# Performance work log

Measured on AMD Instinct MI355X. Metric: run time of the kernel, lower is better.

## Reference

```python
import jax, jax.numpy as jnp
import numpy as np

K = 512
DIM = 256
BETA = 0.25


def setup_inputs() -> dict:
    key = jax.random.key(0)
    k1, k2 = jax.random.split(key)
    x = jax.random.normal(k1, (64, DIM, 32, 32), dtype=jnp.float32)
    lookup_table = jax.random.normal(k2, (K, DIM), dtype=jnp.float32)
    return {"x": x, "lookup_table": lookup_table}


def reference(x, lookup_table):
    b, d, h, w = x.shape
    # [b,d,h,w] -> [b*h*w, d]
    xf = jnp.transpose(x, (0, 2, 3, 1)).reshape(-1, d)
    # Squared Euclidean distances (argmin identical to torch.cdist argmin)
    d2 = (
        jnp.sum(xf * xf, axis=-1, keepdims=True)
        - 2.0 * (xf @ lookup_table.T)
        + jnp.sum(lookup_table * lookup_table, axis=-1)
    )  # [N, K]
    q = jnp.argmin(d2, axis=1)  # [N]
    x_e = lookup_table[q].reshape(b, h, w, d).transpose(0, 3, 1, 2)  # [b,d,h,w]
    q_x = q.reshape(b, h, w)
    codebook_loss = jnp.mean(jnp.square(jax.lax.stop_gradient(x) - x_e))
    commitment_loss = jnp.mean(jnp.square(x - jax.lax.stop_gradient(x_e)))
    loss = codebook_loss + BETA * commitment_loss
    return x_e, q_x, loss
```

## Files before the change

### kernel.cpp

```cpp
#include <hip/hip_runtime.h>

#define DIM     256
#define HW      1024
#define N_ROWS  65536
#define NT      512
#define QBM     128
#define NBLK    512
#define MARGIN  0.0625f

#define OUT_Q_OFF    16777216
#define OUT_LOSS_OFF 16842752

#define WS_DIST   512
#define WS_X2     1024
#define WS_CNT_I  1536
#define WS_LIST_I 2048
#define WS_LUTBF_B 524288

typedef __attribute__((ext_vector_type(8))) short short8v;
typedef __attribute__((ext_vector_type(4))) float floatx4;

__device__ __forceinline__ unsigned short bf16_rne(float f) {
    unsigned int u = __float_as_uint(f);
    u += 0x7fffu + ((u >> 16) & 1u);
    return (unsigned short)(u >> 16);
}
__device__ __forceinline__ float bf16_to_f(unsigned short h) {
    return __uint_as_float(((unsigned int)h) << 16);
}
__device__ __forceinline__ uint4 pack8(const unsigned short* h) {
    uint4 u;
    u.x = (unsigned)h[0] | ((unsigned)h[1] << 16);
    u.y = (unsigned)h[2] | ((unsigned)h[3] << 16);
    u.z = (unsigned)h[4] | ((unsigned)h[5] << 16);
    u.w = (unsigned)h[6] | ((unsigned)h[7] << 16);
    return u;
}

__global__ void c2_kernel(const float* __restrict__ lut, float* __restrict__ ws) {
    if (threadIdx.x == 0) ((int*)ws)[WS_CNT_I] = 0;
    int t = threadIdx.x;
    for (int k = t; k < 512; k += 256) {
        const float4* row = (const float4*)(lut + (size_t)k * DIM);
        float s = 0.f;
        #pragma unroll 8
        for (int i = 0; i < DIM / 4; ++i) {
            float4 v = row[i];
            s += v.x * v.x + v.y * v.y + v.z * v.z + v.w * v.w;
        }
        ws[k] = s;
    }
}

__global__ void lutprep_kernel(const float* __restrict__ lut, float* __restrict__ ws) {
    int g = blockIdx.x * 256 + threadIdx.x;
    int lane = g & 63;
    int ctg  = (g >> 6) & 31;
    int dcg  = g >> 11;
    int code = ctg * 16 + (lane & 15);
    int d0   = dcg * 32 + (lane >> 4) * 8;
    const float* src = lut + (size_t)code * DIM + d0;
    unsigned short hi[8], lo[8];
    #pragma unroll
    for (int j = 0; j < 8; ++j) {
        float v = src[j];
        unsigned short h = bf16_rne(v);
        hi[j] = h;
        lo[j] = bf16_rne(v - bf16_to_f(h));
    }
    char* dst = (char*)ws + WS_LUTBF_B + (size_t)((dcg * 32 + ctg) * 2) * 1024 + lane * 16;
    *(uint4*)dst          = pack8(hi);
    *(uint4*)(dst + 1024) = pack8(lo);
}

__global__ __launch_bounds__(NT, 2) void vq_kernel(const float* __restrict__ x,
                                                   const float* __restrict__ lut,
                                                   float* __restrict__ out,
                                                   float* __restrict__ ws) {
    __shared__ uint4 aS4[1024];
    __shared__ float c2s[512];
    __shared__ float redv1[4][QBM];
    __shared__ float redv2[4][QBM];
    __shared__ int   redi1[4][QBM];
    __shared__ int   qsh[QBM];
    __shared__ float wsumd[2];
    __shared__ float wsumx[8];

    char* aS = (char*)aS4;
    const char* lutbf = (const char*)ws + WS_LUTBF_B;

    const int tid = threadIdx.x;
    const int blk = blockIdx.x;
    const int n0  = blk * QBM;
    const int b   = n0 >> 10;
    const int hw0 = n0 & 1023;
    const float* xb = x + (size_t)b * (DIM * HW) + hw0;

    for (int k = tid; k < 512; k += NT) c2s[k] = ws[k];

    const int wave = tid >> 6;
    const int lane = tid & 63;
    const int l15  = lane & 15;
    const int l4   = lane >> 4;
    const int rg   = wave >> 2;
    const int cg   = wave & 3;

    const int srow   = tid & 127;
    const int schunk = tid >> 7;
    const int srt    = srow >> 4;
    const int slf    = schunk * 16 + (srow & 15);

    float x2local = 0.f;
    floatx4 acc[4][8];
    #pragma unroll
    for (int i = 0; i < 4; ++i)
        #pragma unroll
        for (int j = 0; j < 8; ++j) acc[i][j] = (floatx4)0.f;

    for (int dc = 0; dc < 8; ++dc) {
        __syncthreads();
        {
            const float* src = xb + (size_t)(dc * 32 + schunk * 8) * HW + srow;
            unsigned short hi[8], lo[8];
            #pragma unroll
            for (int j = 0; j < 8; ++j) {
                float v = src[(size_t)j * HW];
                x2local = fmaf(v, v, x2local);
                unsigned short h = bf16_rne(v);
                hi[j] = h;
                lo[j] = bf16_rne(v - bf16_to_f(h));
            }
            *(uint4*)(aS + srt * 1024 + slf * 16)        = pack8(hi);
            *(uint4*)(aS + 8192 + srt * 1024 + slf * 16) = pack8(lo);
        }
        __syncthreads();
        short8v ah[4], al[4];
        #pragma unroll
        for (int rtl = 0; rtl < 4; ++rtl) {
            ah[rtl] = *(const short8v*)(aS + (rg * 4 + rtl) * 1024 + lane * 16);
            al[rtl] = *(const short8v*)(aS + 8192 + (rg * 4 + rtl) * 1024 + lane * 16);
        }
        #pragma unroll
        for (int ct = 0; ct < 8; ++ct) {
            const char* bp = lutbf + (size_t)((dc * 32 + cg * 8 + ct) * 2) * 1024 + lane * 16;
            short8v bh = *(const short8v*)bp;
            short8v bl = *(const short8v*)(bp + 1024);
            #pragma unroll
            for (int rtl = 0; rtl < 4; ++rtl) {
                acc[rtl][ct] = __builtin_amdgcn_mfma_f32_16x16x32_bf16(ah[rtl], bh, acc[rtl][ct], 0, 0, 0);
                acc[rtl][ct] = __builtin_amdgcn_mfma_f32_16x16x32_bf16(al[rtl], bh, acc[rtl][ct], 0, 0, 0);
                acc[rtl][ct] = __builtin_amdgcn_mfma_f32_16x16x32_bf16(ah[rtl], bl, acc[rtl][ct], 0, 0, 0);
            }
        }
    }

    #pragma unroll
    for (int rtl = 0; rtl < 4; ++rtl) {
        #pragma unroll
        for (int r = 0; r < 4; ++r) {
            float v1 = 3.4e38f, v2 = 3.4e38f; int i1 = 0;
            #pragma unroll
            for (int ct = 0; ct < 8; ++ct) {
                int code = cg * 128 + ct * 16 + l15;
                float dist = fmaf(-2.f, acc[rtl][ct][r], c2s[code]);
                if (dist < v1) { v2 = v1; v1 = dist; i1 = code; }
                else if (dist < v2) v2 = dist;
            }
            #pragma unroll
            for (int off = 1; off < 16; off <<= 1) {
                float ov1 = __shfl_xor(v1, off, 64);
                int   oi1 = __shfl_xor(i1, off, 64);
                float ov2 = __shfl_xor(v2, off, 64);
                float nv2 = fminf(fmaxf(v1, ov1), fminf(v2, ov2));
                if (ov1 < v1 || (ov1 == v1 && oi1 < i1)) { v1 = ov1; i1 = oi1; }
                v2 = nv2;
            }
            if (l15 == 0) {
                int row = rg * 64 + rtl * 16 + l4 * 4 + r;
                redv1[cg][row] = v1; redi1[cg][row] = i1; redv2[cg][row] = v2;
            }
        }
    }
    __syncthreads();

    float dist_part = 0.f;
    if (tid < QBM) {
        const int row = tid;
        float v1 = redv1[0][row]; int i1 = redi1[0][row]; float v2 = redv2[0][row];
        #pragma unroll
        for (int s = 1; s < 4; ++s) {
            float ov1 = redv1[s][row]; int oi1 = redi1[s][row]; float ov2 = redv2[s][row];
            float nv2 = fminf(fmaxf(v1, ov1), fminf(v2, ov2));
            if (ov1 < v1 || (ov1 == v1 && oi1 < i1)) { v1 = ov1; i1 = oi1; }
            v2 = nv2;
        }
        qsh[row] = i1;
        out[OUT_Q_OFF + n0 + row] = (float)i1;
        if (v2 - v1 <= MARGIN) {
            int idx = atomicAdd((int*)ws + WS_CNT_I, 1);
            ((int*)ws)[WS_LIST_I + idx] = n0 + row;
        }
        dist_part = v1;
    }

    float dv = dist_part;
    #pragma unroll
    for (int off = 32; off; off >>= 1) dv += __shfl_down(dv, off, 64);
    if (lane == 0 && wave < 2) wsumd[wave] = dv;
    float xv = x2local;
    #pragma unroll
    for (int off = 32; off; off >>= 1) xv += __shfl_down(xv, off, 64);
    if (lane == 0) wsumx[wave] = xv;
    __syncthreads();
    if (tid == 0) {
        float xs = 0.f;
        #pragma unroll
        for (int w = 0; w < 8; ++w) xs += wsumx[w];
        ws[WS_DIST + blk] = wsumd[0] + wsumd[1];
        ws[WS_X2 + blk]   = xs;
    }

    {
        const int row = tid & 127;
        const int dg  = tid >> 7;
        const int q   = qsh[row];
        const float* crow = lut + (size_t)q * DIM;
        float* ob = out + (size_t)b * (DIM * HW) + hw0 + row;
        #pragma unroll 4
        for (int i = 0; i < 16; ++i) {
            int d0 = dg * 64 + i * 4;
            float4 c = *(const float4*)(crow + d0);
            ob[(size_t)(d0 + 0) * HW] = c.x;
            ob[(size_t)(d0 + 1) * HW] = c.y;
            ob[(size_t)(d0 + 2) * HW] = c.z;
            ob[(size_t)(d0 + 3) * HW] = c.w;
        }
    }
}

__global__ void exact_kernel(const float* __restrict__ x, const float* __restrict__ lut,
                             float* __restrict__ out, const float* __restrict__ ws) {
    __shared__ float xr[DIM];
    __shared__ float rv[256];
    __shared__ int   ri[256];
    const int cnt = ((const int*)ws)[WS_CNT_I];
    const int* list = (const int*)ws + WS_LIST_I;
    const int tid = threadIdx.x;
    for (int ii = blockIdx.x; ii < cnt; ii += gridDim.x) {
        const int row = list[ii];
        const int b = row >> 10, hw = row & 1023;
        __syncthreads();
        xr[tid] = x[(size_t)b * (DIM * HW) + (size_t)tid * HW + hw];
        __syncthreads();
        float bv = 3.4e38f; int bi = 0;
        #pragma unroll
        for (int k2 = 0; k2 < 2; ++k2) {
            int k = tid + k2 * 256;
            const float* cr = lut + (size_t)k * DIM;
            float dot = 0.f;
            for (int d = 0; d < DIM; ++d) dot = fmaf(xr[d], cr[d], dot);
            float dist = fmaf(-2.f, dot, ws[k]);
            if (dist < bv || (dist == bv && k < bi)) { bv = dist; bi = k; }
        }
        rv[tid] = bv; ri[tid] = bi;
        __syncthreads();
        for (int s = 128; s; s >>= 1) {
            if (tid < s) {
                float ov = rv[tid + s]; int oi = ri[tid + s];
                if (ov < rv[tid] || (ov == rv[tid] && oi < ri[tid])) {
                    rv[tid] = ov; ri[tid] = oi;
                }
            }
            __syncthreads();
        }
        const int q = ri[0];
        if (tid == 0) out[OUT_Q_OFF + row] = (float)q;
        out[(size_t)b * (DIM * HW) + (size_t)tid * HW + hw] = lut[(size_t)q * DIM + tid];
    }
}

__global__ void loss_kernel(float* __restrict__ out, const float* __restrict__ ws) {
    __shared__ float wsum[4];
    int tid = threadIdx.x;
    float s = 0.f;
    for (int i = tid; i < 1024; i += 256) s += ws[WS_DIST + i];
    #pragma unroll
    for (int off = 32; off; off >>= 1) s += __shfl_down(s, off, 64);
    if ((tid & 63) == 0) wsum[tid >> 6] = s;
    __syncthreads();
    if (tid == 0) {
        float total = wsum[0] + wsum[1] + wsum[2] + wsum[3];
        out[OUT_LOSS_OFF] = total * (1.25f / 16777216.f);
    }
}

extern "C" void kernel_launch(void* const* d_in, const int* in_sizes, int n_in,
                              void* d_out, int out_size, void* d_ws, size_t ws_size,
                              hipStream_t stream) {
    const float* x   = (const float*)d_in[0];
    const float* lut = (const float*)d_in[1];
    float* out = (float*)d_out;
    float* ws  = (float*)d_ws;

    c2_kernel<<<1, 256, 0, stream>>>(lut, ws);
    lutprep_kernel<<<64, 256, 0, stream>>>(lut, ws);
    vq_kernel<<<NBLK, NT, 0, stream>>>(x, lut, out, ws);
    exact_kernel<<<2048, 256, 0, stream>>>(x, lut, out, ws);
    loss_kernel<<<1, 256, 0, stream>>>(out, ws);
}
```

Baseline: 151.0 us.

## Double-buffer x tile in LDS and prefetch next chunk during MFMA

Adds a second LDS buffer for the split-bf16 x tile. The global loads for the next 32-dim chunk are issued before the current chunk's MFMAs, and the conversion and store happen afterwards, which removes one barrier per iteration. All eight codebook B fragments are also loaded into registers up front instead of inside the loop. The goal is to hide global memory latency behind the matrix work, at the cost of more registers and LDS, which may lower occupancy at 2 blocks per CU.

```diff
diff --git a/kernel.cpp b/kernel.cpp
--- a/kernel.cpp
+++ b/kernel.cpp
@@ -77,7 +77,7 @@
                                                    const float* __restrict__ lut,
                                                    float* __restrict__ out,
                                                    float* __restrict__ ws) {
-    __shared__ uint4 aS4[1024];
+    __shared__ char aS[2][16384];
     __shared__ float c2s[512];
     __shared__ float redv1[4][QBM];
     __shared__ float redv2[4][QBM];
@@ -86,7 +86,6 @@
     __shared__ float wsumd[2];
     __shared__ float wsumx[8];
 
-    char* aS = (char*)aS4;
     const char* lutbf = (const char*)ws + WS_LUTBF_B;
 
     const int tid = threadIdx.x;
@@ -109,6 +108,8 @@
     const int schunk = tid >> 7;
     const int srt    = srow >> 4;
     const int slf    = schunk * 16 + (srow & 15);
+    char* awr_hi0 = &aS[0][srt * 1024 + slf * 16];
+    char* awr_hi1 = &aS[1][srt * 1024 + slf * 16];
 
     float x2local = 0.f;
     floatx4 acc[4][8];
@@ -117,40 +118,67 @@
         #pragma unroll
         for (int j = 0; j < 8; ++j) acc[i][j] = (floatx4)0.f;
 
+    {
+        const float* src = xb + (size_t)(schunk * 8) * HW + srow;
+        unsigned short hi[8], lo[8];
+        #pragma unroll
+        for (int j = 0; j < 8; ++j) {
+            float v = src[(size_t)j * HW];
+            x2local = fmaf(v, v, x2local);
+            unsigned short h = bf16_rne(v);
+            hi[j] = h;
+            lo[j] = bf16_rne(v - bf16_to_f(h));
+        }
+        *(uint4*)awr_hi0          = pack8(hi);
+        *(uint4*)(awr_hi0 + 8192) = pack8(lo);
+    }
+    __syncthreads();
+
     for (int dc = 0; dc < 8; ++dc) {
-        __syncthreads();
-        {
-            const float* src = xb + (size_t)(dc * 32 + schunk * 8) * HW + srow;
+        const int cur = dc & 1;
+        float xn[8];
+        if (dc < 7) {
+            const float* src = xb + (size_t)((dc + 1) * 32 + schunk * 8) * HW + srow;
+            #pragma unroll
+            for (int j = 0; j < 8; ++j) xn[j] = src[(size_t)j * HW];
+        }
+        short8v ah[4], al[4];
+        #pragma unroll
+        for (int rtl = 0; rtl < 4; ++rtl) {
+            const char* ra = &aS[cur][(rg * 4 + rtl) * 1024 + lane * 16];
+            ah[rtl] = *(const short8v*)ra;
+            al[rtl] = *(const short8v*)(ra + 8192);
+        }
+        short8v bh[8], bl[8];
+        #pragma unroll
+        for (int ct = 0; ct < 8; ++ct) {
+            const char* bp = lutbf + (size_t)((dc * 32 + cg * 8 + ct) * 2) * 1024 + lane * 16;
+            bh[ct] = *(const short8v*)bp;
+            bl[ct] = *(const short8v*)(bp + 1024);
+        }
+        #pragma unroll
+        for (int ct = 0; ct < 8; ++ct) {
+            #pragma unroll
+            for (int rtl = 0; rtl < 4; ++rtl) {
+                acc[rtl][ct] = __builtin_amdgcn_mfma_f32_16x16x32_bf16(ah[rtl], bh[ct], acc[rtl][ct], 0, 0, 0);
+                acc[rtl][ct] = __builtin_amdgcn_mfma_f32_16x16x32_bf16(al[rtl], bh[ct], acc[rtl][ct], 0, 0, 0);
+                acc[rtl][ct] = __builtin_amdgcn_mfma_f32_16x16x32_bf16(ah[rtl], bl[ct], acc[rtl][ct], 0, 0, 0);
+            }
+        }
+        if (dc < 7) {
             unsigned short hi[8], lo[8];
             #pragma unroll
             for (int j = 0; j < 8; ++j) {
-                float v = src[(size_t)j * HW];
+                float v = xn[j];
                 x2local = fmaf(v, v, x2local);
                 unsigned short h = bf16_rne(v);
                 hi[j] = h;
                 lo[j] = bf16_rne(v - bf16_to_f(h));
             }
-            *(uint4*)(aS + srt * 1024 + slf * 16)        = pack8(hi);
-            *(uint4*)(aS + 8192 + srt * 1024 + slf * 16) = pack8(lo);
-        }
-        __syncthreads();
-        short8v ah[4], al[4];
-        #pragma unroll
-        for (int rtl = 0; rtl < 4; ++rtl) {
-            ah[rtl] = *(const short8v*)(aS + (rg * 4 + rtl) * 1024 + lane * 16);
-            al[rtl] = *(const short8v*)(aS + 8192 + (rg * 4 + rtl) * 1024 + lane * 16);
-        }
-        #pragma unroll
-        for (int ct = 0; ct < 8; ++ct) {
-            const char* bp = lutbf + (size_t)((dc * 32 + cg * 8 + ct) * 2) * 1024 + lane * 16;
-            short8v bh = *(const short8v*)bp;
-            short8v bl = *(const short8v*)(bp + 1024);
-            #pragma unroll
-            for (int rtl = 0; rtl < 4; ++rtl) {
-                acc[rtl][ct] = __builtin_amdgcn_mfma_f32_16x16x32_bf16(ah[rtl], bh, acc[rtl][ct], 0, 0, 0);
-                acc[rtl][ct] = __builtin_amdgcn_mfma_f32_16x16x32_bf16(al[rtl], bh, acc[rtl][ct], 0, 0, 0);
-                acc[rtl][ct] = __builtin_amdgcn_mfma_f32_16x16x32_bf16(ah[rtl], bl, acc[rtl][ct], 0, 0, 0);
-            }
+            char* wr = cur ? awr_hi0 : awr_hi1;
+            *(uint4*)wr          = pack8(hi);
+            *(uint4*)(wr + 8192) = pack8(lo);
+            __syncthreads();
         }
     }
 
```

Result: faster. 147.4 us (-2.4%).

## Stage full x tile in LDS once and double-buffer LUT fragments per wave

Applied to the files above, without the earlier changes.

The VQ kernel now uses 64-row blocks of 256 threads. Each block converts its entire 64x256 x tile to bf16 hi/lo pairs in dynamic LDS (about 68 KB) behind a single barrier, replacing the eight barrier-separated chunk loads. Each wave covers 128 codes in two passes of 64, which halves the live accumulators. It prefetches the next d-chunk's LUT fragments from global into a register double buffer and keeps the code norms in registers. The aim is fewer barriers and less register pressure, but the large LDS footprint caps blocks per CU and lowers occupancy; the block and exact-kernel grid sizes change to match.

```diff
diff --git a/kernel.cpp b/kernel.cpp
--- a/kernel.cpp
+++ b/kernel.cpp
@@ -3,19 +3,21 @@
 #define DIM     256
 #define HW      1024
 #define N_ROWS  65536
-#define NT      512
-#define QBM     128
-#define NBLK    512
+#define NT      256
+#define QBM     64
+#define NBLK    1024
 #define MARGIN  0.0625f
 
 #define OUT_Q_OFF    16777216
 #define OUT_LOSS_OFF 16842752
 
 #define WS_DIST   512
-#define WS_X2     1024
-#define WS_CNT_I  1536
-#define WS_LIST_I 2048
+#define WS_X2     1536
+#define WS_CNT_I  3072
+#define WS_LIST_I 4096
 #define WS_LUTBF_B 524288
+
+#define VQ_LDS 69632
 
 typedef __attribute__((ext_vector_type(8))) short short8v;
 typedef __attribute__((ext_vector_type(4))) float floatx4;
@@ -55,9 +57,9 @@
 __global__ void lutprep_kernel(const float* __restrict__ lut, float* __restrict__ ws) {
     int g = blockIdx.x * 256 + threadIdx.x;
     int lane = g & 63;
-    int ctg  = (g >> 6) & 31;
+    int ctu  = (g >> 6) & 31;
     int dcg  = g >> 11;
-    int code = ctg * 16 + (lane & 15);
+    int code = ctu * 16 + (lane & 15);
     int d0   = dcg * 32 + (lane >> 4) * 8;
     const float* src = lut + (size_t)code * DIM + d0;
     unsigned short hi[8], lo[8];
@@ -68,7 +70,7 @@
         hi[j] = h;
         lo[j] = bf16_rne(v - bf16_to_f(h));
     }
-    char* dst = (char*)ws + WS_LUTBF_B + (size_t)((dcg * 32 + ctg) * 2) * 1024 + lane * 16;
+    char* dst = (char*)ws + WS_LUTBF_B + (size_t)((dcg * 32 + ctu) * 2) * 1024 + lane * 16;
     *(uint4*)dst          = pack8(hi);
     *(uint4*)(dst + 1024) = pack8(lo);
 }
@@ -77,16 +79,13 @@
                                                    const float* __restrict__ lut,
                                                    float* __restrict__ out,
                                                    float* __restrict__ ws) {
-    __shared__ uint4 aS4[1024];
-    __shared__ float c2s[512];
-    __shared__ float redv1[4][QBM];
-    __shared__ float redv2[4][QBM];
-    __shared__ int   redi1[4][QBM];
-    __shared__ int   qsh[QBM];
-    __shared__ float wsumd[2];
-    __shared__ float wsumx[8];
-
-    char* aS = (char*)aS4;
+    extern __shared__ char smem[];
+    float* redv1 = (float*)(smem + 65536);
+    float* redv2 = (float*)(smem + 66560);
+    int*   redi1 = (int*)(smem + 67584);
+    int*   qsh   = (int*)(smem + 68608);
+    float* wsumx = (float*)(smem + 68864);
+
     const char* lutbf = (const char*)ws + WS_LUTBF_B;
 
     const int tid = threadIdx.x;
@@ -96,88 +95,127 @@
     const int hw0 = n0 & 1023;
     const float* xb = x + (size_t)b * (DIM * HW) + hw0;
 
-    for (int k = tid; k < 512; k += NT) c2s[k] = ws[k];
-
     const int wave = tid >> 6;
     const int lane = tid & 63;
     const int l15  = lane & 15;
     const int l4   = lane >> 4;
-    const int rg   = wave >> 2;
-    const int cg   = wave & 3;
-
-    const int srow   = tid & 127;
-    const int schunk = tid >> 7;
-    const int srt    = srow >> 4;
-    const int slf    = schunk * 16 + (srow & 15);
-
+    const int cg   = wave;
+
+    float c2reg[2][4];
+    #pragma unroll
+    for (int ctg = 0; ctg < 2; ++ctg)
+        #pragma unroll
+        for (int ct = 0; ct < 4; ++ct)
+            c2reg[ctg][ct] = ws[(cg * 8 + ctg * 4 + ct) * 16 + l15];
+
+    const int srow = tid & 63;
+    const int sdg  = tid >> 6;
     float x2local = 0.f;
-    floatx4 acc[4][8];
-    #pragma unroll
-    for (int i = 0; i < 4; ++i)
-        #pragma unroll
-        for (int j = 0; j < 8; ++j) acc[i][j] = (floatx4)0.f;
-
-    for (int dc = 0; dc < 8; ++dc) {
-        __syncthreads();
-        {
-            const float* src = xb + (size_t)(dc * 32 + schunk * 8) * HW + srow;
-            unsigned short hi[8], lo[8];
-            #pragma unroll
-            for (int j = 0; j < 8; ++j) {
-                float v = src[(size_t)j * HW];
-                x2local = fmaf(v, v, x2local);
-                unsigned short h = bf16_rne(v);
-                hi[j] = h;
-                lo[j] = bf16_rne(v - bf16_to_f(h));
-            }
-            *(uint4*)(aS + srt * 1024 + slf * 16)        = pack8(hi);
-            *(uint4*)(aS + 8192 + srt * 1024 + slf * 16) = pack8(lo);
-        }
-        __syncthreads();
-        short8v ah[4], al[4];
+    #pragma unroll
+    for (int jj = 0; jj < 8; ++jj) {
+        const int d0 = sdg * 64 + jj * 8;
+        unsigned short hi[8], lo[8];
+        #pragma unroll
+        for (int e = 0; e < 8; ++e) {
+            float v = xb[(size_t)(d0 + e) * HW + srow];
+            x2local = fmaf(v, v, x2local);
+            unsigned short h = bf16_rne(v);
+            hi[e] = h;
+            lo[e] = bf16_rne(v - bf16_to_f(h));
+        }
+        const int dc = d0 >> 5, doct = (d0 >> 3) & 3, rt = srow >> 4;
+        char* basep = smem + (size_t)((rt * 8 + dc) * 2) * 1024 + (doct * 16 + (srow & 15)) * 16;
+        *(uint4*)basep          = pack8(hi);
+        *(uint4*)(basep + 1024) = pack8(lo);
+    }
+    __syncthreads();
+
+    for (int ctg = 0; ctg < 2; ++ctg) {
+        const int ctu0 = cg * 8 + ctg * 4;
+        floatx4 acc[4][4];
+        #pragma unroll
+        for (int i = 0; i < 4; ++i)
+            #pragma unroll
+            for (int j = 0; j < 4; ++j) acc[i][j] = (floatx4)0.f;
+
+        short8v bh0[4], bl0[4], bh1[4], bl1[4];
+        #pragma unroll
+        for (int ct = 0; ct < 4; ++ct) {
+            const char* bp = lutbf + (size_t)((ctu0 + ct) * 2) * 1024 + lane * 16;
+            bh0[ct] = *(const short8v*)bp;
+            bl0[ct] = *(const short8v*)(bp + 1024);
+        }
+        #pragma unroll
+        for (int dc = 0; dc < 8; ++dc) {
+            if (dc < 7) {
+                #pragma unroll
+                for (int ct = 0; ct < 4; ++ct) {
+                    const char* bp = lutbf + (size_t)(((dc + 1) * 32 + ctu0 + ct) * 2) * 1024 + lane * 16;
+                    if ((dc & 1) == 0) { bh1[ct] = *(const short8v*)bp; bl1[ct] = *(const short8v*)(bp + 1024); }
+                    else               { bh0[ct] = *(const short8v*)bp; bl0[ct] = *(const short8v*)(bp + 1024); }
+                }
+            }
+            short8v ah[4], al[4];
+            #pragma unroll
+            for (int rtl = 0; rtl < 4; ++rtl) {
+                const char* ra = smem + (size_t)((rtl * 8 + dc) * 2) * 1024 + lane * 16;
+                ah[rtl] = *(const short8v*)ra;
+                al[rtl] = *(const short8v*)(ra + 1024);
+            }
+            #pragma unroll
+            for (int ct = 0; ct < 4; ++ct) {
+                short8v bh = (dc & 1) ? bh1[ct] : bh0[ct];
+                #pragma unroll
+                for (int rtl = 0; rtl < 4; ++rtl)
+                    acc[rtl][ct] = __builtin_amdgcn_mfma_f32_16x16x32_bf16(ah[rtl], bh, acc[rtl][ct], 0, 0, 0);
+            }
+            #pragma unroll
+            for (int ct = 0; ct < 4; ++ct) {
+                short8v bh = (dc & 1) ? bh1[ct] : bh0[ct];
+                #pragma unroll
+                for (int rtl = 0; rtl < 4; ++rtl)
+                    acc[rtl][ct] = __builtin_amdgcn_mfma_f32_16x16x32_bf16(al[rtl], bh, acc[rtl][ct], 0, 0, 0);
+            }
+            #pragma unroll
+            for (int ct = 0; ct < 4; ++ct) {
+                short8v bl = (dc & 1) ? bl1[ct] : bl0[ct];
+                #pragma unroll
+                for (int rtl = 0; rtl < 4; ++rtl)
+                    acc[rtl][ct] = __builtin_amdgcn_mfma_f32_16x16x32_bf16(ah[rtl], bl, acc[rtl][ct], 0, 0, 0);
+            }
+        }
         #pragma unroll
         for (int rtl = 0; rtl < 4; ++rtl) {
-            ah[rtl] = *(const short8v*)(aS + (rg * 4 + rtl) * 1024 + lane * 16);
-            al[rtl] = *(const short8v*)(aS + 8192 + (rg * 4 + rtl) * 1024 + lane * 16);
-        }
-        #pragma unroll
-        for (int ct = 0; ct < 8; ++ct) {
-            const char* bp = lutbf + (size_t)((dc * 32 + cg * 8 + ct) * 2) * 1024 + lane * 16;
-            short8v bh = *(const short8v*)bp;
-            short8v bl = *(const short8v*)(bp + 1024);
-            #pragma unroll
-            for (int rtl = 0; rtl < 4; ++rtl) {
-                acc[rtl][ct] = __builtin_amdgcn_mfma_f32_16x16x32_bf16(ah[rtl], bh, acc[rtl][ct], 0, 0, 0);
-                acc[rtl][ct] = __builtin_amdgcn_mfma_f32_16x16x32_bf16(al[rtl], bh, acc[rtl][ct], 0, 0, 0);
-                acc[rtl][ct] = __builtin_amdgcn_mfma_f32_16x16x32_bf16(ah[rtl], bl, acc[rtl][ct], 0, 0, 0);
-            }
-        }
-    }
-
-    #pragma unroll
-    for (int rtl = 0; rtl < 4; ++rtl) {
-        #pragma unroll
-        for (int r = 0; r < 4; ++r) {
-            float v1 = 3.4e38f, v2 = 3.4e38f; int i1 = 0;
-            #pragma unroll
-            for (int ct = 0; ct < 8; ++ct) {
-                int code = cg * 128 + ct * 16 + l15;
-                float dist = fmaf(-2.f, acc[rtl][ct][r], c2s[code]);
-                if (dist < v1) { v2 = v1; v1 = dist; i1 = code; }
-                else if (dist < v2) v2 = dist;
-            }
-            #pragma unroll
-            for (int off = 1; off < 16; off <<= 1) {
-                float ov1 = __shfl_xor(v1, off, 64);
-                int   oi1 = __shfl_xor(i1, off, 64);
-                float ov2 = __shfl_xor(v2, off, 64);
-                float nv2 = fminf(fmaxf(v1, ov1), fminf(v2, ov2));
-                if (ov1 < v1 || (ov1 == v1 && oi1 < i1)) { v1 = ov1; i1 = oi1; }
-                v2 = nv2;
-            }
-            if (l15 == 0) {
-                int row = rg * 64 + rtl * 16 + l4 * 4 + r;
-                redv1[cg][row] = v1; redi1[cg][row] = i1; redv2[cg][row] = v2;
+            #pragma unroll
+            for (int r = 0; r < 4; ++r) {
+                float v1 = 3.4e38f, v2 = 3.4e38f; int i1 = 0;
+                #pragma unroll
+                for (int ct = 0; ct < 4; ++ct) {
+                    int code = (ctu0 + ct) * 16 + l15;
+                    float dist = fmaf(-2.f, acc[rtl][ct][r], c2reg[ctg][ct]);
+                    if (dist < v1) { v2 = v1; v1 = dist; i1 = code; }
+                    else if (dist < v2) v2 = dist;
+                }
+                #pragma unroll
+                for (int off = 1; off < 16; off <<= 1) {
+                    float ov1 = __shfl_xor(v1, off, 64);
+                    int   oi1 = __shfl_xor(i1, off, 64);
+                    float ov2 = __shfl_xor(v2, off, 64);
+                    float nv2 = fminf(fmaxf(v1, ov1), fminf(v2, ov2));
+                    if (ov1 < v1 || (ov1 == v1 && oi1 < i1)) { v1 = ov1; i1 = oi1; }
+                    v2 = nv2;
+                }
+                if (l15 == 0) {
+                    int idx = cg * 64 + rtl * 16 + l4 * 4 + r;
+                    if (ctg == 0) {
+                        redv1[idx] = v1; redi1[idx] = i1; redv2[idx] = v2;
+                    } else {
+                        float ov1 = redv1[idx]; float ov2 = redv2[idx];
+                        float nv2 = fminf(fmaxf(v1, ov1), fminf(v2, ov2));
+                        if (v1 < ov1) { redv1[idx] = v1; redi1[idx] = i1; }
+                        redv2[idx] = nv2;
+                    }
+                }
             }
         }
     }
@@ -186,10 +224,10 @@
     float dist_part = 0.f;
     if (tid < QBM) {
         const int row = tid;
-        float v1 = redv1[0][row]; int i1 = redi1[0][row]; float v2 = redv2[0][row];
+        float v1 = redv1[row]; int i1 = redi1[row]; float v2 = redv2[row];
         #pragma unroll
         for (int s = 1; s < 4; ++s) {
-            float ov1 = redv1[s][row]; int oi1 = redi1[s][row]; float ov2 = redv2[s][row];
+            float ov1 = redv1[s * 64 + row]; int oi1 = redi1[s * 64 + row]; float ov2 = redv2[s * 64 + row];
             float nv2 = fminf(fmaxf(v1, ov1), fminf(v2, ov2));
             if (ov1 < v1 || (ov1 == v1 && oi1 < i1)) { v1 = ov1; i1 = oi1; }
             v2 = nv2;
@@ -202,27 +240,21 @@
         }
         dist_part = v1;
     }
-
     float dv = dist_part;
     #pragma unroll
     for (int off = 32; off; off >>= 1) dv += __shfl_down(dv, off, 64);
-    if (lane == 0 && wave < 2) wsumd[wave] = dv;
+    if (tid == 0) ws[WS_DIST + blk] = dv;
+
     float xv = x2local;
     #pragma unroll
     for (int off = 32; off; off >>= 1) xv += __shfl_down(xv, off, 64);
     if (lane == 0) wsumx[wave] = xv;
     __syncthreads();
-    if (tid == 0) {
-        float xs = 0.f;
-        #pragma unroll
-        for (int w = 0; w < 8; ++w) xs += wsumx[w];
-        ws[WS_DIST + blk] = wsumd[0] + wsumd[1];
-        ws[WS_X2 + blk]   = xs;
-    }
+    if (tid == 0) ws[WS_X2 + blk] = wsumx[0] + wsumx[1] + wsumx[2] + wsumx[3];
 
     {
-        const int row = tid & 127;
-        const int dg  = tid >> 7;
+        const int row = tid & 63;
+        const int dg  = tid >> 6;
         const int q   = qsh[row];
         const float* crow = lut + (size_t)q * DIM;
         float* ob = out + (size_t)b * (DIM * HW) + hw0 + row;
@@ -283,7 +315,7 @@
     __shared__ float wsum[4];
     int tid = threadIdx.x;
     float s = 0.f;
-    for (int i = tid; i < 1024; i += 256) s += ws[WS_DIST + i];
+    for (int i = tid; i < 2048; i += 256) s += ws[WS_DIST + i];
     #pragma unroll
     for (int off = 32; off; off >>= 1) s += __shfl_down(s, off, 64);
     if ((tid & 63) == 0) wsum[tid >> 6] = s;
@@ -302,9 +334,12 @@
     float* out = (float*)d_out;
     float* ws  = (float*)d_ws;
 
+    (void)hipFuncSetAttribute((const void*)vq_kernel,
+                              hipFuncAttributeMaxDynamicSharedMemorySize, VQ_LDS);
+
     c2_kernel<<<1, 256, 0, stream>>>(lut, ws);
     lutprep_kernel<<<64, 256, 0, stream>>>(lut, ws);
-    vq_kernel<<<NBLK, NT, 0, stream>>>(x, lut, out, ws);
-    exact_kernel<<<2048, 256, 0, stream>>>(x, lut, out, ws);
+    vq_kernel<<<NBLK, NT, VQ_LDS, stream>>>(x, lut, out, ws);
+    exact_kernel<<<1024, 256, 0, stream>>>(x, lut, out, ws);
     loss_kernel<<<1, 256, 0, stream>>>(out, ws);
 }
```

New measurement: 295.0 us. +95.3%, slower.
